# Kernel tuning notes

Measured on AMD Instinct MI355X. Metric: run time of the kernel, lower is better.

## Reference

```python
import jax, jax.numpy as jnp
import numpy as np

ALPHA = 0.5
SMOOTHING = 0.1
B, C = 16384, 4096


def setup_inputs() -> dict:
    key = jax.random.key(0)
    k1, k2 = jax.random.split(key)
    y_h = jax.random.normal(k1, (B, C), dtype=jnp.float32)
    # y acts as a score matrix; argmax over classes yields the hard label
    y = jax.random.normal(k2, (B, C), dtype=jnp.float32)
    # supervise buffer: smoothing/(C-1) off-diagonal, 1-smoothing on diagonal
    supervise = jnp.full((C, C), SMOOTHING / (C - 1), dtype=jnp.float32)
    supervise = supervise.at[jnp.arange(C), jnp.arange(C)].set(1.0 - SMOOTHING)
    return {"y_h": y_h, "y": y, "supervise": supervise}


def reference(y_h, y, supervise):
    n_classes = supervise.shape[0]
    y_idx = jnp.argmax(y, axis=1)                      # [B] hard labels
    log_p = jax.nn.log_softmax(y_h, axis=-1)           # [B, C]
    probs = jnp.exp(log_p)                             # [B, C]

    # ---- step(): no-grad buffer update (training mode) ----
    pred = jnp.argmax(probs, axis=-1)                  # [B]
    mask = (pred == y_idx)                             # correctly classified
    probs_c = probs * mask[:, None].astype(probs.dtype)
    # update.index_add_(1, pred[mask], probs[mask].T): scatter-add rows of
    # probs into column `pred` of the [C, C] update matrix (dup indices ok)
    update = jnp.zeros((n_classes, n_classes), probs.dtype).at[:, pred].add(probs_c.T)
    idx_count = jnp.zeros((n_classes,), probs.dtype).at[pred].add(mask.astype(probs.dtype))

    # ---- soft loss: gather supervise columns by label ----
    true_dist = supervise.T[y_idx]                     # [B, C] == index_select(supervise,1,y).T
    soft_loss = jnp.mean(jnp.sum(-true_dist * log_p, axis=-1))

    # ---- hard loss: standard cross entropy ----
    hard_loss = -jnp.mean(jnp.take_along_axis(log_p, y_idx[:, None], axis=-1))

    loss = ALPHA * hard_loss + (1.0 - ALPHA) * soft_loss
    return loss, update, idx_count
```

## Files before the change

### kernel.cpp

```cpp
#include <hip/hip_runtime.h>
#include <math.h>


constexpr int CC    = 4096;
constexpr int WAVE  = 64;
constexpr int WPB   = 4;
constexpr int TPB   = 256;
constexpr int NCH   = 4;
constexpr int CHUNK = CC / NCH;
constexpr int JPW   = CHUNK / (WAVE * 4);
constexpr float ALPHA_V = 0.5f;
constexpr int ACC_SLOTS = 64;

__device__ inline void amax2(float v, int i, float& bv, int& bi) {
  if (v > bv || (v == bv && i < bi)) { bv = v; bi = i; }
}

__device__ inline void wave_argmax(float& lv, int& li) {
  #pragma unroll
  for (int o = 1; o < WAVE; o <<= 1) {
    float ov = __shfl_xor(lv, o, WAVE);
    int   oi = __shfl_xor(li, o, WAVE);
    amax2(ov, oi, lv, li);
  }
}

__device__ inline float wave_sum(float v) {
  #pragma unroll
  for (int o = 1; o < WAVE; o <<= 1) v += __shfl_xor(v, o, WAVE);
  return v;
}

__global__ void ols_transpose(const float* __restrict__ in,
                              float* __restrict__ supT,
                              float* __restrict__ upd,
                              float* __restrict__ cnt,
                              double* __restrict__ acc,
                              int* __restrict__ mcount, int C) {
  __shared__ float tile[32][33];
  const int bx = blockIdx.x * 32, by = blockIdx.y * 32;
  const int tx = threadIdx.x, ty = threadIdx.y;
  if (blockIdx.y == 0 && ty == 0) cnt[bx + tx] = 0.0f;
  if (blockIdx.x == 0 && blockIdx.y == 0) {
    const int t = ty * 32 + tx;
    if (t == 0) *mcount = 0;
    if (t < ACC_SLOTS * 2) acc[t] = 0.0;
  }
  #pragma unroll
  for (int j = 0; j < 32; j += 8)
    tile[ty + j][tx] = in[(size_t)(by + ty + j) * C + bx + tx];
  __syncthreads();
  #pragma unroll
  for (int j = 0; j < 32; j += 8) {
    const size_t o = (size_t)(bx + ty + j) * C + by + tx;
    supT[o] = tile[tx][ty + j];
    upd[o]  = 0.0f;
  }
}

__global__ void ols_part_y(const float* __restrict__ y,
                           float* __restrict__ ypmax,
                           int* __restrict__ ypidx) {
  const int wv = threadIdx.x >> 6, lane = threadIdx.x & 63;
  const int task = blockIdx.x * WPB + wv;
  const int b = task >> 2, ch = task & 3;
  const float4* p = reinterpret_cast<const float4*>(y + (size_t)b * CC + ch * CHUNK);

  float4 v[JPW];
  #pragma unroll
  for (int j = 0; j < JPW; ++j) v[j] = p[j * WAVE + lane];

  float m = -INFINITY; int mi = 0x7fffffff;
  #pragma unroll
  for (int j = 0; j < JPW; ++j) {
    const int base = ch * CHUNK + (j * WAVE + lane) * 4;
    amax2(v[j].x, base + 0, m, mi);
    amax2(v[j].y, base + 1, m, mi);
    amax2(v[j].z, base + 2, m, mi);
    amax2(v[j].w, base + 3, m, mi);
  }
  wave_argmax(m, mi);
  if (lane == 0) { ypmax[task] = m; ypidx[task] = mi; }
}

__global__ void ols_part_x(const float* __restrict__ y_h,
                           const float* __restrict__ supT,
                           const float* __restrict__ ypmax,
                           const int* __restrict__ ypidx,
                           float* __restrict__ xpmax, int* __restrict__ xpidx,
                           float* __restrict__ xpse, float* __restrict__ xpW,
                           float* __restrict__ xpWX) {
  const int wv = threadIdx.x >> 6, lane = threadIdx.x & 63;
  const int task = blockIdx.x * WPB + wv;
  const int b = task >> 2, ch = task & 3;

  const float4 ym = reinterpret_cast<const float4*>(ypmax)[b];
  const int4   yi = reinterpret_cast<const int4*>(ypidx)[b];
  float lm = ym.x; int lab = yi.x;
  amax2(ym.y, yi.y, lm, lab);
  amax2(ym.z, yi.z, lm, lab);
  amax2(ym.w, yi.w, lm, lab);

  const float4* px = reinterpret_cast<const float4*>(y_h + (size_t)b * CC + ch * CHUNK);
  const float4* pw = reinterpret_cast<const float4*>(supT + (size_t)lab * CC + ch * CHUNK);

  float4 xv[JPW], wv4[JPW];
  #pragma unroll
  for (int j = 0; j < JPW; ++j) xv[j] = px[j * WAVE + lane];
  #pragma unroll
  for (int j = 0; j < JPW; ++j) wv4[j] = pw[j * WAVE + lane];

  float m = -INFINITY; int mi = 0x7fffffff;
  float se = 0.f, W = 0.f, WX = 0.f;
  #pragma unroll
  for (int j = 0; j < JPW; ++j) {
    const int base = ch * CHUNK + (j * WAVE + lane) * 4;
    amax2(xv[j].x, base + 0, m, mi);
    amax2(xv[j].y, base + 1, m, mi);
    amax2(xv[j].z, base + 2, m, mi);
    amax2(xv[j].w, base + 3, m, mi);
    se += __expf(xv[j].x) + __expf(xv[j].y) + __expf(xv[j].z) + __expf(xv[j].w);
    W  += wv4[j].x + wv4[j].y + wv4[j].z + wv4[j].w;
    WX += wv4[j].x * xv[j].x + wv4[j].y * xv[j].y
        + wv4[j].z * xv[j].z + wv4[j].w * xv[j].w;
  }
  wave_argmax(m, mi);
  se = wave_sum(se);
  W  = wave_sum(W);
  WX = wave_sum(WX);
  if (lane == 0) {
    xpmax[task] = m; xpidx[task] = mi;
    xpse[task] = se; xpW[task] = W; xpWX[task] = WX;
  }
}

__global__ void ols_rowfin(const float* __restrict__ y_h,
                           const float* __restrict__ ypmax, const int* __restrict__ ypidx,
                           const float* __restrict__ xpmax, const int* __restrict__ xpidx,
                           const float* __restrict__ xpse, const float* __restrict__ xpW,
                           const float* __restrict__ xpWX,
                           float* __restrict__ Zbuf,
                           int2* __restrict__ matches, int* __restrict__ mcount,
                           float* __restrict__ cnt, double* __restrict__ acc) {
  const int b = blockIdx.x * TPB + threadIdx.x;

  const float4 ym = reinterpret_cast<const float4*>(ypmax)[b];
  const int4   yi = reinterpret_cast<const int4*>(ypidx)[b];
  float lm = ym.x; int lab = yi.x;
  amax2(ym.y, yi.y, lm, lab);
  amax2(ym.z, yi.z, lm, lab);
  amax2(ym.w, yi.w, lm, lab);

  const float4 xm = reinterpret_cast<const float4*>(xpmax)[b];
  const int4   xi = reinterpret_cast<const int4*>(xpidx)[b];
  float pm = xm.x; int pred = xi.x;
  amax2(xm.y, xi.y, pm, pred);
  amax2(xm.z, xi.z, pm, pred);
  amax2(xm.w, xi.w, pm, pred);

  const float4 se4 = reinterpret_cast<const float4*>(xpse)[b];
  const float4 W4  = reinterpret_cast<const float4*>(xpW)[b];
  const float4 WX4 = reinterpret_cast<const float4*>(xpWX)[b];
  const float Z  = se4.x + se4.y + se4.z + se4.w;
  const float W  = W4.x + W4.y + W4.z + W4.w;
  const float WX = WX4.x + WX4.y + WX4.z + WX4.w;

  const float logZ = __logf(Z);
  const float xl   = y_h[(size_t)b * CC + lab];
  float soft = logZ * W - WX;
  float hard = logZ - xl;
  Zbuf[b] = Z;

  if (pred == lab) {
    const int pos = atomicAdd(mcount, 1);
    matches[pos] = make_int2(b, pred);
    atomicAdd(&cnt[pred], 1.0f);
  }

  hard = wave_sum(hard);
  soft = wave_sum(soft);
  if ((threadIdx.x & 63) == 0) {
    const int slot = ((b >> 6) & (ACC_SLOTS - 1)) * 2;
    atomicAdd(&acc[slot + 0], (double)hard);
    atomicAdd(&acc[slot + 1], (double)soft);
  }
}

__global__ void ols_scatter(const float* __restrict__ y_h,
                            const int2* __restrict__ matches,
                            const int* __restrict__ mcount,
                            const float* __restrict__ Zbuf,
                            float* __restrict__ upd,
                            const double* __restrict__ acc,
                            float* __restrict__ out0, double invB) {
  if (blockIdx.x == 0 && threadIdx.x == 0) {
    double h = 0.0, s = 0.0;
    for (int i = 0; i < ACC_SLOTS; ++i) { h += acc[i * 2]; s += acc[i * 2 + 1]; }
    out0[0] = (float)(((double)ALPHA_V * h + (1.0 - (double)ALPHA_V) * s) * invB);
  }
  const int n = *mcount;
  for (int i = blockIdx.x; i < n; i += gridDim.x) {
    const int2 mr = matches[i];
    const int b = mr.x, pred = mr.y;
    const float invZ = 1.0f / Zbuf[b];
    const float4* px = reinterpret_cast<const float4*>(y_h + (size_t)b * CC);
    #pragma unroll
    for (int j = 0; j < 4; ++j) {
      const int i4 = j * TPB + threadIdx.x;
      const float4 xv = px[i4];
      const int base = i4 * 4;
      atomicAdd(&upd[(size_t)(base + 0) * CC + pred], __expf(xv.x) * invZ);
      atomicAdd(&upd[(size_t)(base + 1) * CC + pred], __expf(xv.y) * invZ);
      atomicAdd(&upd[(size_t)(base + 2) * CC + pred], __expf(xv.z) * invZ);
      atomicAdd(&upd[(size_t)(base + 3) * CC + pred], __expf(xv.w) * invZ);
    }
  }
}

__global__ void ols_fallback(const float* __restrict__ y_h, const float* __restrict__ y,
                             const float* __restrict__ sup,
                             float* __restrict__ upd, float* __restrict__ cnt,
                             double* __restrict__ acc) {
  const int wv = threadIdx.x >> 6, lane = threadIdx.x & 63;
  const int b = blockIdx.x * WPB + wv;
  const size_t roff = (size_t)b * CC;
  const float4* y4 = reinterpret_cast<const float4*>(y + roff);
  const float4* x4 = reinterpret_cast<const float4*>(y_h + roff);
  const int K16 = CC / (WAVE * 4);

  float lv = -INFINITY; int li = 0x7fffffff;
  for (int k = 0; k < K16; ++k) {
    const float4 v = y4[k * WAVE + lane];
    const int base = (k * WAVE + lane) * 4;
    amax2(v.x, base + 0, lv, li); amax2(v.y, base + 1, lv, li);
    amax2(v.z, base + 2, lv, li); amax2(v.w, base + 3, lv, li);
  }
  wave_argmax(lv, li);
  const int lab = li;
  const float xl = y_h[roff + lab];

  float m = -INFINITY; int mi = 0x7fffffff;
  float se = 0.f, W = 0.f, WX = 0.f;
  for (int k = 0; k < K16; ++k) {
    const float4 xv = x4[k * WAVE + lane];
    const int base = (k * WAVE + lane) * 4;
    const float w0 = sup[(size_t)(base + 0) * CC + lab];
    const float w1 = sup[(size_t)(base + 1) * CC + lab];
    const float w2 = sup[(size_t)(base + 2) * CC + lab];
    const float w3 = sup[(size_t)(base + 3) * CC + lab];
    amax2(xv.x, base + 0, m, mi); amax2(xv.y, base + 1, m, mi);
    amax2(xv.z, base + 2, m, mi); amax2(xv.w, base + 3, m, mi);
    se += __expf(xv.x) + __expf(xv.y) + __expf(xv.z) + __expf(xv.w);
    W  += w0 + w1 + w2 + w3;
    WX += w0 * xv.x + w1 * xv.y + w2 * xv.z + w3 * xv.w;
  }
  wave_argmax(m, mi);
  const int pred = mi;
  const float Z = wave_sum(se), Wt = wave_sum(W), WXt = wave_sum(WX);
  const float logZ = __logf(Z);
  if (pred == lab) {
    const float invZ = 1.0f / Z;
    for (int k = 0; k < K16; ++k) {
      const float4 xv = x4[k * WAVE + lane];
      const int base = (k * WAVE + lane) * 4;
      atomicAdd(&upd[(size_t)(base + 0) * CC + pred], __expf(xv.x) * invZ);
      atomicAdd(&upd[(size_t)(base + 1) * CC + pred], __expf(xv.y) * invZ);
      atomicAdd(&upd[(size_t)(base + 2) * CC + pred], __expf(xv.z) * invZ);
      atomicAdd(&upd[(size_t)(base + 3) * CC + pred], __expf(xv.w) * invZ);
    }
    if (lane == 0) atomicAdd(&cnt[pred], 1.0f);
  }
  if (lane == 0) {
    const int slot = (b & (ACC_SLOTS - 1)) * 2;
    atomicAdd(&acc[slot + 0], (double)(logZ - xl));
    atomicAdd(&acc[slot + 1], (double)(logZ * Wt - WXt));
  }
}

__global__ void ols_finalize(const double* __restrict__ acc,
                             float* __restrict__ out, double invB) {
  double h = 0.0, s = 0.0;
  for (int i = 0; i < ACC_SLOTS; ++i) { h += acc[i * 2]; s += acc[i * 2 + 1]; }
  out[0] = (float)(((double)ALPHA_V * h + (1.0 - (double)ALPHA_V) * s) * invB);
}

extern "C" void kernel_launch(void* const* d_in, const int* in_sizes, int n_in,
                              void* d_out, int out_size, void* d_ws, size_t ws_size,
                              hipStream_t stream) {
  const float* y_h = (const float*)d_in[0];
  const float* y   = (const float*)d_in[1];
  const float* sup = (const float*)d_in[2];
  const int C = CC;
  const int B = in_sizes[0] / C;

  float* out        = (float*)d_out;
  float* out_update = out + 1;
  float* out_count  = out + 1 + (size_t)C * C;

  char* ws = (char*)d_ws;
  double* acc    = (double*)ws;
  int*    mcount = (int*)(ws + 1024);
  float*  Zbuf   = (float*)(ws + 4096);
  int2*   matches= (int2*)(ws + 69632);
  float*  ypmax  = (float*)(ws + 200704);
  int*    ypidx  = (int*)  (ws + 462848);
  float*  xpmax  = (float*)(ws + 724992);
  int*    xpidx  = (int*)  (ws + 987136);
  float*  xpse   = (float*)(ws + 1249280);
  float*  xpW    = (float*)(ws + 1511424);
  float*  xpWX   = (float*)(ws + 1773568);
  float*  supT   = (float*)(ws + 2035712);
  const size_t need = 2035712 + (size_t)C * C * sizeof(float);

  if (ws_size >= need) {
    dim3 g(C / 32, C / 32), bl(32, 8);
    ols_transpose<<<g, bl, 0, stream>>>(sup, supT, out_update, out_count,
                                        acc, mcount, C);
    ols_part_y<<<B * NCH / WPB, TPB, 0, stream>>>(y, ypmax, ypidx);
    ols_part_x<<<B * NCH / WPB, TPB, 0, stream>>>(y_h, supT, ypmax, ypidx,
                                                  xpmax, xpidx, xpse, xpW, xpWX);
    ols_rowfin<<<B / TPB, TPB, 0, stream>>>(y_h, ypmax, ypidx,
                                            xpmax, xpidx, xpse, xpW, xpWX,
                                            Zbuf, matches, mcount,
                                            out_count, acc);
    ols_scatter<<<64, TPB, 0, stream>>>(y_h, matches, mcount, Zbuf,
                                        out_update, acc, out, 1.0 / (double)B);
  } else {
    hipMemsetAsync(d_out, 0, (size_t)out_size * sizeof(float), stream);
    hipMemsetAsync(d_ws, 0, 4096, stream);
    ols_fallback<<<B / WPB, TPB, 0, stream>>>(y_h, y, sup,
                                              out_update, out_count, acc);
    ols_finalize<<<1, 1, 0, stream>>>(acc, out, 1.0 / (double)B);
  }
}
```

Baseline: 209.2 us.

## Fuse transpose with label argmax and fold scatter into row-finalize kernel

The supervise transpose/zeroing kernel and the per-row label argmax kernel are merged into one launch that uses even blocks for transpose tiles and odd blocks for y-chunk argmax, so the two memory-bound phases can overlap. The global match list and separate scatter kernel are removed. Each row-finalize block now collects its matching rows in shared memory and scatters their probabilities into the update matrix itself, with a slow per-thread fallback when a block has more than 32 matches. This cuts launches and the Zbuf/matches round trip, but the scatter now runs across 64 blocks interleaved with row finalisation and adds a single-thread finalize launch.

```diff
diff --git a/kernel.cpp b/kernel.cpp
--- a/kernel.cpp
+++ b/kernel.cpp
@@ -11,6 +11,7 @@
 constexpr int JPW   = CHUNK / (WAVE * 4);
 constexpr float ALPHA_V = 0.5f;
 constexpr int ACC_SLOTS = 64;
+constexpr int MCAP  = 32;
 
 __device__ inline void amax2(float v, int i, float& bv, int& bi) {
   if (v > bv || (v == bv && i < bi)) { bv = v; bi = i; }
@@ -31,56 +32,55 @@
   return v;
 }
 
-__global__ void ols_transpose(const float* __restrict__ in,
-                              float* __restrict__ supT,
-                              float* __restrict__ upd,
-                              float* __restrict__ cnt,
-                              double* __restrict__ acc,
-                              int* __restrict__ mcount, int C) {
+__global__ void ols_mega(const float* __restrict__ sup,
+                         float* __restrict__ supT,
+                         float* __restrict__ upd,
+                         float* __restrict__ cnt,
+                         double* __restrict__ acc,
+                         const float* __restrict__ y,
+                         float* __restrict__ ypmax,
+                         int* __restrict__ ypidx, int C) {
   __shared__ float tile[32][33];
-  const int bx = blockIdx.x * 32, by = blockIdx.y * 32;
-  const int tx = threadIdx.x, ty = threadIdx.y;
-  if (blockIdx.y == 0 && ty == 0) cnt[bx + tx] = 0.0f;
-  if (blockIdx.x == 0 && blockIdx.y == 0) {
-    const int t = ty * 32 + tx;
-    if (t == 0) *mcount = 0;
-    if (t < ACC_SLOTS * 2) acc[t] = 0.0;
-  }
-  #pragma unroll
-  for (int j = 0; j < 32; j += 8)
-    tile[ty + j][tx] = in[(size_t)(by + ty + j) * C + bx + tx];
-  __syncthreads();
-  #pragma unroll
-  for (int j = 0; j < 32; j += 8) {
-    const size_t o = (size_t)(bx + ty + j) * C + by + tx;
-    supT[o] = tile[tx][ty + j];
-    upd[o]  = 0.0f;
-  }
-}
-
-__global__ void ols_part_y(const float* __restrict__ y,
-                           float* __restrict__ ypmax,
-                           int* __restrict__ ypidx) {
-  const int wv = threadIdx.x >> 6, lane = threadIdx.x & 63;
-  const int task = blockIdx.x * WPB + wv;
-  const int b = task >> 2, ch = task & 3;
-  const float4* p = reinterpret_cast<const float4*>(y + (size_t)b * CC + ch * CHUNK);
-
-  float4 v[JPW];
-  #pragma unroll
-  for (int j = 0; j < JPW; ++j) v[j] = p[j * WAVE + lane];
-
-  float m = -INFINITY; int mi = 0x7fffffff;
-  #pragma unroll
-  for (int j = 0; j < JPW; ++j) {
-    const int base = ch * CHUNK + (j * WAVE + lane) * 4;
-    amax2(v[j].x, base + 0, m, mi);
-    amax2(v[j].y, base + 1, m, mi);
-    amax2(v[j].z, base + 2, m, mi);
-    amax2(v[j].w, base + 3, m, mi);
-  }
-  wave_argmax(m, mi);
-  if (lane == 0) { ypmax[task] = m; ypidx[task] = mi; }
+  const int blk = blockIdx.x;
+  if ((blk & 1) == 0) {
+    const int tid = threadIdx.x;
+    const int t2 = blk >> 1;
+    const int bx = (t2 & 127) * 32, by = (t2 >> 7) * 32;
+    const int tx = tid & 31, ty = tid >> 5;
+    if (by == 0 && ty == 0) cnt[bx + tx] = 0.0f;
+    if (t2 == 0 && tid < ACC_SLOTS * 2) acc[tid] = 0.0;
+    #pragma unroll
+    for (int j = 0; j < 32; j += 8)
+      tile[ty + j][tx] = sup[(size_t)(by + ty + j) * C + bx + tx];
+    __syncthreads();
+    #pragma unroll
+    for (int j = 0; j < 32; j += 8) {
+      const size_t o = (size_t)(bx + ty + j) * C + by + tx;
+      supT[o] = tile[tx][ty + j];
+      upd[o]  = 0.0f;
+    }
+  } else {
+    const int wv = threadIdx.x >> 6, lane = threadIdx.x & 63;
+    const int task = (blk >> 1) * WPB + wv;
+    const int b = task >> 2, ch = task & 3;
+    const float4* p = reinterpret_cast<const float4*>(y + (size_t)b * CC + ch * CHUNK);
+
+    float4 v[JPW];
+    #pragma unroll
+    for (int j = 0; j < JPW; ++j) v[j] = p[j * WAVE + lane];
+
+    float m = -INFINITY; int mi = 0x7fffffff;
+    #pragma unroll
+    for (int j = 0; j < JPW; ++j) {
+      const int base = ch * CHUNK + (j * WAVE + lane) * 4;
+      amax2(v[j].x, base + 0, m, mi);
+      amax2(v[j].y, base + 1, m, mi);
+      amax2(v[j].z, base + 2, m, mi);
+      amax2(v[j].w, base + 3, m, mi);
+    }
+    wave_argmax(m, mi);
+    if (lane == 0) { ypmax[task] = m; ypidx[task] = mi; }
+  }
 }
 
 __global__ void ols_part_x(const float* __restrict__ y_h,
@@ -139,10 +139,15 @@
                            const float* __restrict__ xpmax, const int* __restrict__ xpidx,
                            const float* __restrict__ xpse, const float* __restrict__ xpW,
                            const float* __restrict__ xpWX,
-                           float* __restrict__ Zbuf,
-                           int2* __restrict__ matches, int* __restrict__ mcount,
+                           float* __restrict__ upd,
                            float* __restrict__ cnt, double* __restrict__ acc) {
-  const int b = blockIdx.x * TPB + threadIdx.x;
+  __shared__ int   s_n;
+  __shared__ int   s_row[MCAP];
+  __shared__ int   s_pred[MCAP];
+  __shared__ float s_invZ[MCAP];
+  const int tid = threadIdx.x;
+  const int b = blockIdx.x * TPB + tid;
+  if (tid == 0) s_n = 0;
 
   const float4 ym = reinterpret_cast<const float4*>(ypmax)[b];
   const int4   yi = reinterpret_cast<const int4*>(ypidx)[b];
@@ -169,52 +174,54 @@
   const float xl   = y_h[(size_t)b * CC + lab];
   float soft = logZ * W - WX;
   float hard = logZ - xl;
-  Zbuf[b] = Z;
-
+
+  __syncthreads();
+  bool overflow = false;
   if (pred == lab) {
-    const int pos = atomicAdd(mcount, 1);
-    matches[pos] = make_int2(b, pred);
+    const int pos = atomicAdd(&s_n, 1);
+    if (pos < MCAP) { s_row[pos] = b; s_pred[pos] = pred; s_invZ[pos] = 1.0f / Z; }
+    else overflow = true;
     atomicAdd(&cnt[pred], 1.0f);
+  }
+  if (overflow) {
+    const float invZ = 1.0f / Z;
+    const float* xr = y_h + (size_t)b * CC;
+    for (int c = 0; c < CC; ++c)
+      atomicAdd(&upd[(size_t)c * CC + pred], __expf(xr[c]) * invZ);
   }
 
   hard = wave_sum(hard);
   soft = wave_sum(soft);
-  if ((threadIdx.x & 63) == 0) {
+  if ((tid & 63) == 0) {
     const int slot = ((b >> 6) & (ACC_SLOTS - 1)) * 2;
     atomicAdd(&acc[slot + 0], (double)hard);
     atomicAdd(&acc[slot + 1], (double)soft);
   }
-}
-
-__global__ void ols_scatter(const float* __restrict__ y_h,
-                            const int2* __restrict__ matches,
-                            const int* __restrict__ mcount,
-                            const float* __restrict__ Zbuf,
-                            float* __restrict__ upd,
-                            const double* __restrict__ acc,
-                            float* __restrict__ out0, double invB) {
-  if (blockIdx.x == 0 && threadIdx.x == 0) {
-    double h = 0.0, s = 0.0;
-    for (int i = 0; i < ACC_SLOTS; ++i) { h += acc[i * 2]; s += acc[i * 2 + 1]; }
-    out0[0] = (float)(((double)ALPHA_V * h + (1.0 - (double)ALPHA_V) * s) * invB);
-  }
-  const int n = *mcount;
-  for (int i = blockIdx.x; i < n; i += gridDim.x) {
-    const int2 mr = matches[i];
-    const int b = mr.x, pred = mr.y;
-    const float invZ = 1.0f / Zbuf[b];
-    const float4* px = reinterpret_cast<const float4*>(y_h + (size_t)b * CC);
+
+  __syncthreads();
+  const int n = min(s_n, MCAP);
+  for (int i = 0; i < n; ++i) {
+    const int rb = s_row[i], p = s_pred[i];
+    const float iz = s_invZ[i];
+    const float4* px = reinterpret_cast<const float4*>(y_h + (size_t)rb * CC);
     #pragma unroll
     for (int j = 0; j < 4; ++j) {
-      const int i4 = j * TPB + threadIdx.x;
+      const int i4 = j * TPB + tid;
       const float4 xv = px[i4];
       const int base = i4 * 4;
-      atomicAdd(&upd[(size_t)(base + 0) * CC + pred], __expf(xv.x) * invZ);
-      atomicAdd(&upd[(size_t)(base + 1) * CC + pred], __expf(xv.y) * invZ);
-      atomicAdd(&upd[(size_t)(base + 2) * CC + pred], __expf(xv.z) * invZ);
-      atomicAdd(&upd[(size_t)(base + 3) * CC + pred], __expf(xv.w) * invZ);
+      atomicAdd(&upd[(size_t)(base + 0) * CC + p], __expf(xv.x) * iz);
+      atomicAdd(&upd[(size_t)(base + 1) * CC + p], __expf(xv.y) * iz);
+      atomicAdd(&upd[(size_t)(base + 2) * CC + p], __expf(xv.z) * iz);
+      atomicAdd(&upd[(size_t)(base + 3) * CC + p], __expf(xv.w) * iz);
     }
   }
+}
+
+__global__ void ols_finalize(const double* __restrict__ acc,
+                             float* __restrict__ out, double invB) {
+  double h = 0.0, s = 0.0;
+  for (int i = 0; i < ACC_SLOTS; ++i) { h += acc[i * 2]; s += acc[i * 2 + 1]; }
+  out[0] = (float)(((double)ALPHA_V * h + (1.0 - (double)ALPHA_V) * s) * invB);
 }
 
 __global__ void ols_fallback(const float* __restrict__ y_h, const float* __restrict__ y,
@@ -277,13 +284,6 @@
   }
 }
 
-__global__ void ols_finalize(const double* __restrict__ acc,
-                             float* __restrict__ out, double invB) {
-  double h = 0.0, s = 0.0;
-  for (int i = 0; i < ACC_SLOTS; ++i) { h += acc[i * 2]; s += acc[i * 2 + 1]; }
-  out[0] = (float)(((double)ALPHA_V * h + (1.0 - (double)ALPHA_V) * s) * invB);
-}
-
 extern "C" void kernel_launch(void* const* d_in, const int* in_sizes, int n_in,
                               void* d_out, int out_size, void* d_ws, size_t ws_size,
                               hipStream_t stream) {
@@ -298,33 +298,26 @@
   float* out_count  = out + 1 + (size_t)C * C;
 
   char* ws = (char*)d_ws;
-  double* acc    = (double*)ws;
-  int*    mcount = (int*)(ws + 1024);
-  float*  Zbuf   = (float*)(ws + 4096);
-  int2*   matches= (int2*)(ws + 69632);
-  float*  ypmax  = (float*)(ws + 200704);
-  int*    ypidx  = (int*)  (ws + 462848);
-  float*  xpmax  = (float*)(ws + 724992);
-  int*    xpidx  = (int*)  (ws + 987136);
-  float*  xpse   = (float*)(ws + 1249280);
-  float*  xpW    = (float*)(ws + 1511424);
-  float*  xpWX   = (float*)(ws + 1773568);
-  float*  supT   = (float*)(ws + 2035712);
-  const size_t need = 2035712 + (size_t)C * C * sizeof(float);
+  double* acc   = (double*)ws;
+  float*  ypmax = (float*)(ws + 4096);
+  int*    ypidx = (int*)  (ws + 266240);
+  float*  xpmax = (float*)(ws + 528384);
+  int*    xpidx = (int*)  (ws + 790528);
+  float*  xpse  = (float*)(ws + 1052672);
+  float*  xpW   = (float*)(ws + 1314816);
+  float*  xpWX  = (float*)(ws + 1576960);
+  float*  supT  = (float*)(ws + 1839104);
+  const size_t need = 1839104 + (size_t)C * C * sizeof(float);
 
   if (ws_size >= need) {
-    dim3 g(C / 32, C / 32), bl(32, 8);
-    ols_transpose<<<g, bl, 0, stream>>>(sup, supT, out_update, out_count,
-                                        acc, mcount, C);
-    ols_part_y<<<B * NCH / WPB, TPB, 0, stream>>>(y, ypmax, ypidx);
+    ols_mega<<<32768, TPB, 0, stream>>>(sup, supT, out_update, out_count,
+                                        acc, y, ypmax, ypidx, C);
     ols_part_x<<<B * NCH / WPB, TPB, 0, stream>>>(y_h, supT, ypmax, ypidx,
                                                   xpmax, xpidx, xpse, xpW, xpWX);
     ols_rowfin<<<B / TPB, TPB, 0, stream>>>(y_h, ypmax, ypidx,
                                             xpmax, xpidx, xpse, xpW, xpWX,
-                                            Zbuf, matches, mcount,
-                                            out_count, acc);
-    ols_scatter<<<64, TPB, 0, stream>>>(y_h, matches, mcount, Zbuf,
-                                        out_update, acc, out, 1.0 / (double)B);
+                                            out_update, out_count, acc);
+    ols_finalize<<<1, 1, 0, stream>>>(acc, out, 1.0 / (double)B);
   } else {
     hipMemsetAsync(d_out, 0, (size_t)out_size * sizeof(float), stream);
     hipMemsetAsync(d_ws, 0, 4096, stream);
```

Result: faster. 196.8 us (-5.9%).
